# Performance work log

Hardware: AMD Instinct MI355X
Metric: run time of the kernel (lower is better)

Reference implementation:

```python
import jax, jax.numpy as jnp
import numpy as np

NUM_HEADS = 8
NUM_LEVEL = 4
KERNEL = 2
NUM_POINT = KERNEL * KERNEL
D_MODEL = 256
HEAD_DIM = D_MODEL // NUM_HEADS
REF_SIZE = 4
EPS = 1e-6


def _kernel_indices():
    # even kernel: linspace(-k/2+0.5, k/2-0.5, k) -> [-0.5, 0.5] for k=2
    ind = np.linspace(-KERNEL // 2 + 0.5, KERNEL // 2 - 0.5, KERNEL)
    i, j = np.meshgrid(ind, ind, indexing='ij')
    ki = np.stack([j, i], axis=-1).reshape(-1, 2) / KERNEL  # (P, 2), (x, y)
    return jnp.asarray(ki, dtype=jnp.float32)


def _ref_windows(shapes):
    # mask is None -> centers on a regular grid, size = ref_size / (H, W)
    refs = []
    for (H, W) in shapes:
        y = (jnp.arange(1, H + 1, dtype=jnp.float32) - 0.5) / (H + EPS)
        x = (jnp.arange(1, W + 1, dtype=jnp.float32) - 0.5) / (W + EPS)
        yy, xx = jnp.meshgrid(y, x, indexing='ij')           # (H, W)
        center = jnp.stack([xx, yy], axis=-1).reshape(-1, 2)  # (HW, 2)
        size = jnp.broadcast_to(
            jnp.array([REF_SIZE / W, REF_SIZE / H], dtype=jnp.float32), center.shape)
        refs.append(jnp.concatenate([center, size], axis=-1))
    return jnp.concatenate(refs, axis=0)  # (L, 4)


def _bilinear_sample(vflat, grid, H, W):
    """vflat: (B, H*W, M, D) one level; grid: (B, Lq, M, P, 2) normalized [0,1].
    Returns (B, Lq, M, P, D). Zero padding outside, align_corners=False."""
    B, _, M, D = vflat.shape
    x = grid[..., 0] * W - 0.5
    y = grid[..., 1] * H - 0.5
    x0 = jnp.floor(x); y0 = jnp.floor(y)
    lx = x - x0; ly = y - y0
    x0i = x0.astype(jnp.int32); y0i = y0.astype(jnp.int32)
    bidx = jnp.arange(B)[:, None, None, None]
    midx = jnp.arange(M)[None, None, :, None]

    def corner(xi, yi, w):
        valid = (xi >= 0) & (xi < W) & (yi >= 0) & (yi < H)
        idx = jnp.clip(yi, 0, H - 1) * W + jnp.clip(xi, 0, W - 1)
        g = vflat[bidx, idx, midx]  # (B, Lq, M, P, D)
        return g * (w * valid.astype(w.dtype))[..., None]

    out = corner(x0i, y0i, (1 - lx) * (1 - ly))
    out = out + corner(x0i + 1, y0i, lx * (1 - ly))
    out = out + corner(x0i, y0i + 1, (1 - lx) * ly)
    out = out + corner(x0i + 1, y0i + 1, lx * ly)
    return out


def setup_inputs() -> dict:
    key = jax.random.key(0)
    ks = jax.random.split(key, 20)
    spatial = [(100, 100), (50, 50), (25, 25), (13, 13)]
    B = 4
    inp = {}
    for i, (H, W) in enumerate(spatial):
        inp[f'value{i}'] = jax.random.normal(ks[i], (B, D_MODEL, H, W), dtype=jnp.float32)
        inp[f'pos{i}'] = jax.random.normal(ks[4 + i], (B, D_MODEL, H, W), dtype=jnp.float32)
    s = 0.05
    inp['Wv'] = jax.random.normal(ks[8], (D_MODEL, D_MODEL), dtype=jnp.float32) * s
    inp['bv'] = jnp.zeros((D_MODEL,), dtype=jnp.float32)
    inp['Wo'] = jax.random.normal(ks[9], (D_MODEL, D_MODEL), dtype=jnp.float32) * s
    inp['bo'] = jnp.zeros((D_MODEL,), dtype=jnp.float32)
    nb = NUM_LEVEL * NUM_HEADS * 4
    inp['Wbox'] = jax.random.normal(ks[10], (nb, D_MODEL), dtype=jnp.float32) * s
    inp['bbox'] = jax.random.uniform(ks[11], (nb,), dtype=jnp.float32)
    na = NUM_HEADS * NUM_LEVEL * NUM_POINT
    inp['Wattn'] = jax.random.normal(ks[12], (na, D_MODEL), dtype=jnp.float32) * s
    inp['battn'] = jax.random.normal(ks[13], (na,), dtype=jnp.float32) * s
    return inp


def reference(value0, value1, value2, value3, pos0, pos1, pos2, pos3,
              Wv, bv, Wo, bo, Wbox, bbox, Wattn, battn):
    levels = [value0, value1, value2, value3]
    poss = [pos0, pos1, pos2, pos3]
    shapes = [(v.shape[2], v.shape[3]) for v in levels]
    B = levels[0].shape[0]

    # flatten pyramid: (B, C, H, W) -> (B, HW, C)
    value = jnp.concatenate(
        [v.reshape(B, D_MODEL, -1).transpose(0, 2, 1) for v in levels], axis=1)
    pos = jnp.concatenate(
        [p.reshape(B, D_MODEL, -1).transpose(0, 2, 1) for p in poss], axis=1)
    L = value.shape[1]

    query = value + pos
    vp = (value @ Wv.T + bv).reshape(B, L, NUM_HEADS, HEAD_DIM)

    attn = jax.nn.softmax(
        (query @ Wattn.T + battn).reshape(B, L, NUM_HEADS, NUM_LEVEL * NUM_POINT),
        axis=-1).reshape(B, L, NUM_HEADS, NUM_LEVEL, NUM_POINT)

    offset = (query @ Wbox.T + bbox).reshape(B, L, NUM_HEADS, NUM_LEVEL, 4)
    ref = _ref_windows(shapes)[None, :, None, None, :]          # (1, L, 1, 1, 4)
    boxes = ref + offset / 8.0 * ref[..., jnp.array([2, 3, 2, 3])]
    center = boxes[..., None, :2]                               # (B, L, M, NL, 1, 2)
    size = boxes[..., None, 2:]
    ki = _kernel_indices()[None, None, None, None, :, :]        # (1,1,1,1,P,2)
    grid = center + ki * jax.nn.relu(size)                      # (B, L, M, NL, P, 2)

    out = jnp.zeros((B, L, NUM_HEADS, HEAD_DIM), dtype=vp.dtype)
    start = 0
    for l, (H, W) in enumerate(shapes):
        end = start + H * W
        vf = vp[:, start:end]                                   # (B, HW, M, D)
        sampled = _bilinear_sample(vf, grid[:, :, :, l], H, W)  # (B, L, M, P, D)
        out = out + jnp.einsum('blmp,blmpd->blmd', attn[:, :, :, l], sampled)
        start = end

    return out.reshape(B, L, D_MODEL) @ Wo.T + bo
```

## Files before the change

### kernel.cpp

```cpp
#include <hip/hip_runtime.h>
#include <cstdint>
#include <cmath>

#define D_MODEL 256
#define NH 8
#define NLVL 4
#define LTOT 13294
#define BATCH 4
#define BTOT (BATCH * LTOT)
#define RPAD 53248

typedef __attribute__((ext_vector_type(8))) short bf8;
typedef __attribute__((ext_vector_type(4))) float f4;
typedef __attribute__((ext_vector_type(2))) float f2;

__device__ __forceinline__ unsigned short f2bf(float x) {
    unsigned u = __float_as_uint(x);
    u += 0x7fffu + ((u >> 16) & 1u);
    return (unsigned short)(u >> 16);
}
__device__ __forceinline__ float bf2f(unsigned short h) {
    return __uint_as_float(((unsigned)h) << 16);
}
__device__ __forceinline__ f2 up2(unsigned u) {
    return (f2){__uint_as_float(u << 16), __uint_as_float(u & 0xffff0000u)};
}
__device__ __forceinline__ int swzf(int i, int s) { return s ^ ((i >> 1) & 3); }
__device__ __forceinline__ int xcd_swz(int hw, int nwg) {
    int xcd = hw & 7, k = hw >> 3;
    int q = nwg >> 3, r = nwg & 7;
    return (xcd < r ? xcd * (q + 1) : r * (q + 1) + (xcd - r) * q) + k;
}

__device__ __forceinline__ void level_of(int l, int& lv, int& hw, int& Wl, int& HWl, int& loff) {
    if (l < 10000)      { lv = 0; loff = 0;     Wl = 100; HWl = 10000; }
    else if (l < 12500) { lv = 1; loff = 10000; Wl = 50;  HWl = 2500;  }
    else if (l < 13125) { lv = 2; loff = 12500; Wl = 25;  HWl = 625;   }
    else                { lv = 3; loff = 13125; Wl = 13;  HWl = 169;   }
    hw = l - loff;
}

#define NCONV (RPAD / 64)
#define NPACK 96
#define NGEO  208

__global__ __launch_bounds__(256) void convert_pack(
    const float* __restrict__ v0, const float* __restrict__ v1,
    const float* __restrict__ v2, const float* __restrict__ v3,
    const float* __restrict__ p0, const float* __restrict__ p1,
    const float* __restrict__ p2, const float* __restrict__ p3,
    const float* __restrict__ Wv, const float* __restrict__ Wattn,
    const float* __restrict__ Wbox, const float* __restrict__ Wo,
    unsigned short* __restrict__ Gv, unsigned short* __restrict__ Gq,
    unsigned short* __restrict__ W1hi, unsigned short* __restrict__ W1lo,
    unsigned short* __restrict__ Wohi, unsigned short* __restrict__ Wolo,
    float4* __restrict__ geot) {
    __shared__ unsigned short HV[64][130];
    __shared__ unsigned short HQ[64][130];
    int t = threadIdx.x;

    if (blockIdx.x >= NCONV) {
        if (blockIdx.x >= NCONV + NPACK) {
            int rr = (blockIdx.x - (NCONV + NPACK)) * 256 + t;
            if (rr < BTOT) {
                int l = rr % LTOT;
                int lv, hw, Wl, HWl, loff;
                level_of(l, lv, hw, Wl, HWl, loff);
                int x, y;
                switch (lv) {
                    case 0:  y = hw / 100; x = hw - y * 100; break;
                    case 1:  y = hw / 50;  x = hw - y * 50;  break;
                    case 2:  y = hw / 25;  x = hw - y * 25;  break;
                    default: y = hw / 13;  x = hw - y * 13;  break;
                }
                float denom = (float)((double)Wl + 1e-6);
                float4 g;
                g.x = ((float)x + 0.5f) / denom;
                g.y = ((float)y + 0.5f) / denom;
                g.z = 4.0f / (float)Wl;
                g.w = __int_as_float(rr - l);
                geot[rr] = g;
            }
            return;
        }
        int tid = (blockIdx.x - NCONV) * 256 + t;
        const float* src;
        unsigned short *dh, *dl;
        int nb, kb, j, s;
        if (tid < 16384) {
            nb = tid >> 12; kb = (tid >> 9) & 7; j = (tid >> 2) & 127; s = tid & 3;
            int f = nb * 128 + j, c0 = kb * 32 + s * 8;
            if (f < 256)      src = Wv + (size_t)f * 256 + c0;
            else if (f < 384) src = Wattn + (size_t)(f - 256) * 256 + c0;
            else              src = Wbox + (size_t)(f - 384) * 256 + c0;
            dh = W1hi; dl = W1lo;
        } else {
            int t2 = tid - 16384;
            nb = t2 >> 12; kb = (t2 >> 9) & 7; j = (t2 >> 2) & 127; s = t2 & 3;
            int f = nb * 128 + j, c0 = kb * 32 + s * 8;
            src = Wo + (size_t)f * 256 + c0;
            dh = Wohi; dl = Wolo;
        }
        int base = (((nb * 8 + kb) * 128 + j) * 4 + swzf(j, s)) * 8;
        #pragma unroll
        for (int e = 0; e < 8; ++e) {
            float x = src[e];
            unsigned short h = f2bf(x);
            dh[base + e] = h;
            dl[base + e] = f2bf(x - bf2f(h));
        }
        return;
    }

    int w = t >> 6, lane = t & 63;
    int r0 = blockIdx.x * 64;

    int r = r0 + lane; if (r >= BTOT) r = BTOT - 1;
    int b = r / LTOT, l = r % LTOT;
    int lv, hw, Wl, HWl, loff;
    level_of(l, lv, hw, Wl, HWl, loff);
    const float *vb, *pb;
    switch (lv) { case 0: vb = v0; pb = p0; break; case 1: vb = v1; pb = p1; break;
                  case 2: vb = v2; pb = p2; break; default: vb = v3; pb = p3; break; }
    size_t base = (size_t)b * D_MODEL * (size_t)HWl + (size_t)hw;
    vb += base; pb += base;

    int kb2 = (lane >> 2) & 3, slot = lane & 3;
    for (int h = 0; h < 2; ++h) {
        #pragma unroll 4
        for (int i = 0; i < 32; ++i) {
            int cl = i * 4 + w;
            int c = h * 128 + cl;
            float av = vb[(size_t)c * HWl];
            float aq = av + pb[(size_t)c * HWl];
            HV[lane][cl] = f2bf(av);
            HQ[lane][cl] = f2bf(aq);
        }
        __syncthreads();
        #pragma unroll
        for (int j = 0; j < 8; ++j) {
            int plane = j >> 2;
            int rl = (j & 3) * 16 + w * 4 + (lane >> 4);
            int oct = slot ^ ((rl >> 1) & 3);
            const unsigned* s32 = (const unsigned*)(plane ? &HQ[rl][kb2 * 32 + oct * 8]
                                                          : &HV[rl][kb2 * 32 + oct * 8]);
            uint4 vst = make_uint4(s32[0], s32[1], s32[2], s32[3]);
            unsigned short* dst = (plane ? Gq : Gv)
                + (size_t)(r0 + rl) * 256 + (h * 4 + kb2) * 32 + slot * 8;
            *(uint4*)dst = vst;
        }
        __syncthreads();
    }
}

__global__ __launch_bounds__(512, 4) void gemm1_mfma(
    const unsigned short* __restrict__ Gv, const unsigned short* __restrict__ Gq,
    const unsigned short* __restrict__ W1hi, const unsigned short* __restrict__ W1lo,
    const float* __restrict__ bv, const float* __restrict__ battn, const float* __restrict__ bbox,
    unsigned short* __restrict__ VPb, float* __restrict__ LB) {
    __shared__ __align__(16) unsigned short Ah[2][8192], Bh[2][4096], Bl[2][4096];
    int t = threadIdx.x;
    int lid = xcd_swz(blockIdx.x, 4 * (RPAD / 256));
    int nb = lid & 3;
    int r0 = (lid >> 2) * 256;
    const unsigned short* Asrc = (nb < 2) ? Gv : Gq;
    int w = t >> 6, lane = t & 63;
    int wr = w >> 1, wc = w & 1;
    int row_l = lane & 15, oct = lane >> 4;

    const unsigned short* Bbh = W1hi + (size_t)nb * 32768;
    const unsigned short* Bbl = W1lo + (size_t)nb * 32768;

    f4 acc[4][4];
    #pragma unroll
    for (int i = 0; i < 4; ++i)
        #pragma unroll
        for (int j = 0; j < 4; ++j) acc[i][j] = (f4){0.f, 0.f, 0.f, 0.f};

    int c0 = t, c1 = t + 512;
    const unsigned short* a0b = Asrc + (size_t)(r0 + (c0 >> 2)) * 256 + (c0 & 3) * 8;
    const unsigned short* a1b = Asrc + (size_t)(r0 + (c1 >> 2)) * 256 + (c1 & 3) * 8;

#define G1_STAGE(bb, kb)                                                            \
    {                                                                               \
        __builtin_amdgcn_global_load_lds(a0b + (kb) * 32, &Ah[bb][w * 512], 16, 0, 0);        \
        __builtin_amdgcn_global_load_lds(a1b + (kb) * 32, &Ah[bb][4096 + w * 512], 16, 0, 0); \
        __builtin_amdgcn_global_load_lds(Bbh + (kb) * 4096 + c0 * 8, &Bh[bb][w * 512], 16, 0, 0); \
        __builtin_amdgcn_global_load_lds(Bbl + (kb) * 4096 + c0 * 8, &Bl[bb][w * 512], 16, 0, 0); \
    }

    G1_STAGE(0, 0);
    for (int kb = 0; kb < 8; ++kb) {
        __syncthreads();
        if (kb < 7) G1_STAGE((kb + 1) & 1, kb + 1);
        int bb = kb & 1;
        bf8 a[4], bh[4], bl[4];
        #pragma unroll
        for (int x = 0; x < 4; ++x) {
            int ri = wr * 64 + x * 16 + row_l;
            int ci = wc * 64 + x * 16 + row_l;
            a[x]  = *(const bf8*)(&Ah[bb][ri * 32 + swzf(ri, oct) * 8]);
            bh[x] = *(const bf8*)(&Bh[bb][ci * 32 + swzf(ci, oct) * 8]);
            bl[x] = *(const bf8*)(&Bl[bb][ci * 32 + swzf(ci, oct) * 8]);
        }
        #pragma unroll
        for (int mi = 0; mi < 4; ++mi)
            #pragma unroll
            for (int ni = 0; ni < 4; ++ni) {
                f4 c = acc[mi][ni];
                c = __builtin_amdgcn_mfma_f32_16x16x32_bf16(a[mi], bh[ni], c, 0, 0, 0);
                c = __builtin_amdgcn_mfma_f32_16x16x32_bf16(a[mi], bl[ni], c, 0, 0, 0);
                acc[mi][ni] = c;
            }
    }
    #pragma unroll
    for (int ni = 0; ni < 4; ++ni) {
        int col = wc * 64 + ni * 16 + row_l;
        float bias;
        if (nb == 0) bias = bv[col];
        else if (nb == 1) bias = bv[128 + col];
        else if (nb == 2) bias = battn[col];
        else bias = bbox[col];
        #pragma unroll
        for (int mi = 0; mi < 4; ++mi) {
            #pragma unroll
            for (int v = 0; v < 4; ++v) {
                int rr = r0 + wr * 64 + mi * 16 + oct * 4 + v;
                if (rr < BTOT) {
                    float val = acc[mi][ni][v] + bias;
                    if (nb < 2) VPb[(size_t)rr * 256 + nb * 128 + col] = f2bf(val);
                    else        LB[(size_t)rr * 256 + (nb - 2) * 128 + col] = val;
                }
            }
        }
    }
}

__global__ __launch_bounds__(256) void sampler_kernel(const unsigned short* __restrict__ VPb,
                                                      const float* __restrict__ LB,
                                                      const float4* __restrict__ geot,
                                                      unsigned short* __restrict__ att_hi,
                                                      unsigned short* __restrict__ att_lo) {
    __shared__ float sw[64][128];
    const int Ws2[4]   = {100, 50, 25, 13};
    const int offs2[4] = {0, 10000, 12500, 13125};
    int t = threadIdx.x;
    int blk = xcd_swz(blockIdx.x, (BTOT * NH) / 64);

    #pragma unroll
    for (int pass = 0; pass < 4; ++pass) {
        int g = (t >> 4) + pass * 16;
        int p = t & 15;
        int grp = blk * 64 + g;
        int m = grp & 7;
        int r = grp >> 3;

        float4 gt = geot[r];
        float cx = gt.x, cy = gt.y, rsw = gt.z;
        int rb0 = __float_as_int(gt.w);

        const float* Lrow = LB + (size_t)r * 256;
        float lg = Lrow[m * 16 + p];
        float mx = lg;
        #pragma unroll
        for (int off = 8; off >= 1; off >>= 1)
            mx = fmaxf(mx, __shfl_xor(mx, off, 16));
        float e = __expf(lg - mx);
        float ssum = e;
        #pragma unroll
        for (int off = 8; off >= 1; off >>= 1)
            ssum += __shfl_xor(ssum, off, 16);
        float aw = e / ssum;

        int lp = p >> 2, pp = p & 3;
        int W2 = Ws2[lp];
        float fW2 = (float)W2;
        float o0 = Lrow[128 + m * 16 + lp * 4 + 0];
        float o1 = Lrow[128 + m * 16 + lp * 4 + 1];
        float o2 = Lrow[128 + m * 16 + lp * 4 + 2];
        float o3 = Lrow[128 + m * 16 + lp * 4 + 3];
        float bcx = cx + o0 * 0.125f * rsw;
        float bcy = cy + o1 * 0.125f * rsw;
        float bsx = fmaxf(fmaf(o2 * 0.125f, rsw, rsw), 0.f);
        float bsy = fmaxf(fmaf(o3 * 0.125f, rsw, rsw), 0.f);
        float kx = (pp & 1)  ? 0.25f : -0.25f;
        float ky = (pp >> 1) ? 0.25f : -0.25f;
        float xs = fmaf(bcx + kx * bsx, fW2, -0.5f);
        float ys = fmaf(bcy + ky * bsy, fW2, -0.5f);
        float x0f = floorf(xs), y0f = floorf(ys);
        float lx = xs - x0f, ly = ys - y0f;
        int x0 = (int)x0f, y0 = (int)y0f;
        int x1 = x0 + 1, y1 = y0 + 1;
        bool vx0 = (x0 >= 0) & (x0 < W2), vx1 = (x1 >= 0) & (x1 < W2);
        bool vy0 = (y0 >= 0) & (y0 < W2), vy1 = (y1 >= 0) & (y1 < W2);
        int x0c = min(max(x0, 0), W2 - 1), x1c = min(max(x1, 0), W2 - 1);
        int y0c = min(max(y0, 0), W2 - 1), y1c = min(max(y1, 0), W2 - 1);
        float w00 = (vx0 & vy0) ? aw * (1.f - lx) * (1.f - ly) : 0.f;
        float w01 = (vx1 & vy0) ? aw * lx * (1.f - ly) : 0.f;
        float w10 = (vx0 & vy1) ? aw * (1.f - lx) * ly : 0.f;
        float w11 = (vx1 & vy1) ? aw * lx * ly : 0.f;
        int rowb = rb0 + offs2[lp];
        int col  = m * 32;
        int i00 = ((rowb + y0c * W2 + x0c) * 256 + col) * 2;
        int i01 = ((rowb + y0c * W2 + x1c) * 256 + col) * 2;
        int i10 = ((rowb + y1c * W2 + x0c) * 256 + col) * 2;
        int i11 = ((rowb + y1c * W2 + x1c) * 256 + col) * 2;
        float* dst = &sw[g][(p ^ (g & 3)) << 3];
        *(float4*)dst       = (float4){w00, w01, w10, w11};
        *(float4*)(dst + 4) = (float4){__int_as_float(i00), __int_as_float(i01),
                                       __int_as_float(i10), __int_as_float(i11)};
    }
    __syncthreads();

    int g = t >> 2, lane4 = t & 3;
    unsigned dby = (unsigned)lane4 * 16u;
    const char* Vb = (const char*)VPb;
    f2 a01 = {0.f, 0.f}, a23 = {0.f, 0.f}, a45 = {0.f, 0.f}, a67 = {0.f, 0.f};
    #pragma unroll
    for (int p = 0; p < 16; ++p) {
        const float* sp = &sw[g][(p ^ (g & 3)) << 3];
        float4 wv = *(const float4*)sp;
        float4 fi = *(const float4*)(sp + 4);
        uint4 u00 = *(const uint4*)(Vb + (size_t)(__float_as_uint(fi.x) + dby));
        uint4 u01 = *(const uint4*)(Vb + (size_t)(__float_as_uint(fi.y) + dby));
        uint4 u10 = *(const uint4*)(Vb + (size_t)(__float_as_uint(fi.z) + dby));
        uint4 u11 = *(const uint4*)(Vb + (size_t)(__float_as_uint(fi.w) + dby));
        f2 w0 = {wv.x, wv.x}, w1 = {wv.y, wv.y}, w2 = {wv.z, wv.z}, w3 = {wv.w, wv.w};
        a01 = __builtin_elementwise_fma(w0, up2(u00.x), a01);
        a23 = __builtin_elementwise_fma(w0, up2(u00.y), a23);
        a45 = __builtin_elementwise_fma(w0, up2(u00.z), a45);
        a67 = __builtin_elementwise_fma(w0, up2(u00.w), a67);
        a01 = __builtin_elementwise_fma(w1, up2(u01.x), a01);
        a23 = __builtin_elementwise_fma(w1, up2(u01.y), a23);
        a45 = __builtin_elementwise_fma(w1, up2(u01.z), a45);
        a67 = __builtin_elementwise_fma(w1, up2(u01.w), a67);
        a01 = __builtin_elementwise_fma(w2, up2(u10.x), a01);
        a23 = __builtin_elementwise_fma(w2, up2(u10.y), a23);
        a45 = __builtin_elementwise_fma(w2, up2(u10.z), a45);
        a67 = __builtin_elementwise_fma(w2, up2(u10.w), a67);
        a01 = __builtin_elementwise_fma(w3, up2(u11.x), a01);
        a23 = __builtin_elementwise_fma(w3, up2(u11.y), a23);
        a45 = __builtin_elementwise_fma(w3, up2(u11.z), a45);
        a67 = __builtin_elementwise_fma(w3, up2(u11.w), a67);
    }
    int grp = blk * 64 + g;
    int m2 = grp & 7, r2 = grp >> 3;
    int slot = lane4 ^ ((r2 >> 1) & 3);
    size_t base = (size_t)r2 * 256 + m2 * 32 + slot * 8;
    float av[8] = {a01.x, a01.y, a23.x, a23.y, a45.x, a45.y, a67.x, a67.y};
    unsigned hp[4], lp4[4];
    #pragma unroll
    for (int q = 0; q < 4; ++q) {
        unsigned short h0 = f2bf(av[q * 2]), h1 = f2bf(av[q * 2 + 1]);
        unsigned short l0 = f2bf(av[q * 2] - bf2f(h0)), l1 = f2bf(av[q * 2 + 1] - bf2f(h1));
        hp[q]  = ((unsigned)h1 << 16) | h0;
        lp4[q] = ((unsigned)l1 << 16) | l0;
    }
    *(uint4*)&att_hi[base] = make_uint4(hp[0], hp[1], hp[2], hp[3]);
    *(uint4*)&att_lo[base] = make_uint4(lp4[0], lp4[1], lp4[2], lp4[3]);
}

__global__ __launch_bounds__(512, 2) void gemm2_mfma(
    const unsigned short* __restrict__ Ahi_g, const unsigned short* __restrict__ Alo_g,
    const unsigned short* __restrict__ Wohi, const unsigned short* __restrict__ Wolo,
    const float* __restrict__ bo, float* __restrict__ out) {
    __shared__ __align__(16) unsigned short Ah[2][8192], Al[2][8192], Bh[2][4096], Bl[2][4096];
    int t = threadIdx.x;
    int lid = xcd_swz(blockIdx.x, 2 * (RPAD / 256));
    int nb = lid & 1;
    int r0 = (lid >> 1) * 256;
    int w = t >> 6, lane = t & 63;
    int wr = w >> 1, wc = w & 1;
    int row_l = lane & 15, oct = lane >> 4;

    const unsigned short* Bbh = Wohi + (size_t)nb * 32768;
    const unsigned short* Bbl = Wolo + (size_t)nb * 32768;

    f4 acc[4][4];
    #pragma unroll
    for (int i = 0; i < 4; ++i)
        #pragma unroll
        for (int j = 0; j < 4; ++j) acc[i][j] = (f4){0.f, 0.f, 0.f, 0.f};

    int c0 = t, c1 = t + 512;
    int ra0 = r0 + (c0 >> 2); if (ra0 >= BTOT) ra0 = BTOT - 1;
    int ra1 = r0 + (c1 >> 2); if (ra1 >= BTOT) ra1 = BTOT - 1;
    const unsigned short* ah0 = Ahi_g + (size_t)ra0 * 256 + (c0 & 3) * 8;
    const unsigned short* ah1 = Ahi_g + (size_t)ra1 * 256 + (c1 & 3) * 8;
    const unsigned short* al0 = Alo_g + (size_t)ra0 * 256 + (c0 & 3) * 8;
    const unsigned short* al1 = Alo_g + (size_t)ra1 * 256 + (c1 & 3) * 8;

#define G2_STAGE(bb, kb)                                                            \
    {                                                                               \
        __builtin_amdgcn_global_load_lds(ah0 + (kb) * 32, &Ah[bb][w * 512], 16, 0, 0);        \
        __builtin_amdgcn_global_load_lds(ah1 + (kb) * 32, &Ah[bb][4096 + w * 512], 16, 0, 0); \
        __builtin_amdgcn_global_load_lds(al0 + (kb) * 32, &Al[bb][w * 512], 16, 0, 0);        \
        __builtin_amdgcn_global_load_lds(al1 + (kb) * 32, &Al[bb][4096 + w * 512], 16, 0, 0); \
        __builtin_amdgcn_global_load_lds(Bbh + (kb) * 4096 + c0 * 8, &Bh[bb][w * 512], 16, 0, 0); \
        __builtin_amdgcn_global_load_lds(Bbl + (kb) * 4096 + c0 * 8, &Bl[bb][w * 512], 16, 0, 0); \
    }

    G2_STAGE(0, 0);
    for (int kb = 0; kb < 8; ++kb) {
        __syncthreads();
        if (kb < 7) G2_STAGE((kb + 1) & 1, kb + 1);
        int bb = kb & 1;
        bf8 ah[4], al[4], bh[4], bl[4];
        #pragma unroll
        for (int x = 0; x < 4; ++x) {
            int ri = wr * 64 + x * 16 + row_l;
            int ci = wc * 64 + x * 16 + row_l;
            ah[x] = *(const bf8*)(&Ah[bb][ri * 32 + swzf(ri, oct) * 8]);
            al[x] = *(const bf8*)(&Al[bb][ri * 32 + swzf(ri, oct) * 8]);
            bh[x] = *(const bf8*)(&Bh[bb][ci * 32 + swzf(ci, oct) * 8]);
            bl[x] = *(const bf8*)(&Bl[bb][ci * 32 + swzf(ci, oct) * 8]);
        }
        #pragma unroll
        for (int mi = 0; mi < 4; ++mi)
            #pragma unroll
            for (int ni = 0; ni < 4; ++ni) {
                f4 c = acc[mi][ni];
                c = __builtin_amdgcn_mfma_f32_16x16x32_bf16(ah[mi], bh[ni], c, 0, 0, 0);
                c = __builtin_amdgcn_mfma_f32_16x16x32_bf16(ah[mi], bl[ni], c, 0, 0, 0);
                c = __builtin_amdgcn_mfma_f32_16x16x32_bf16(al[mi], bh[ni], c, 0, 0, 0);
                acc[mi][ni] = c;
            }
    }
    #pragma unroll
    for (int ni = 0; ni < 4; ++ni) {
        int col = wc * 64 + ni * 16 + row_l;
        float bias = bo[nb * 128 + col];
        #pragma unroll
        for (int mi = 0; mi < 4; ++mi) {
            #pragma unroll
            for (int v = 0; v < 4; ++v) {
                int rr = r0 + wr * 64 + mi * 16 + oct * 4 + v;
                if (rr < BTOT)
                    out[(size_t)rr * 256 + nb * 128 + col] = acc[mi][ni][v] + bias;
            }
        }
    }
}

extern "C" void kernel_launch(void* const* d_in, const int* in_sizes, int n_in,
                              void* d_out, int out_size, void* d_ws, size_t ws_size,
                              hipStream_t stream) {
    const float* v0 = (const float*)d_in[0];
    const float* p0 = (const float*)d_in[1];
    const float* v1 = (const float*)d_in[2];
    const float* p1 = (const float*)d_in[3];
    const float* v2 = (const float*)d_in[4];
    const float* p2 = (const float*)d_in[5];
    const float* v3 = (const float*)d_in[6];
    const float* p3 = (const float*)d_in[7];
    const float* Wv    = (const float*)d_in[8];
    const float* bv    = (const float*)d_in[9];
    const float* Wo    = (const float*)d_in[10];
    const float* bo    = (const float*)d_in[11];
    const float* Wbox  = (const float*)d_in[12];
    const float* bbox  = (const float*)d_in[13];
    const float* Wattn = (const float*)d_in[14];
    const float* battn = (const float*)d_in[15];
    float* out = (float*)d_out;

    char* ws = (char*)d_ws;
    unsigned short* W1hi = (unsigned short*)(ws);
    unsigned short* W1lo = (unsigned short*)(ws + 262144);
    unsigned short* Wohi = (unsigned short*)(ws + 524288);
    unsigned short* Wolo = (unsigned short*)(ws + 655360);
    unsigned short* Gv   = (unsigned short*)(ws + 1048576);
    unsigned short* Gq   = (unsigned short*)(ws + 1048576 + 27262976);
    unsigned short* atth = Gv;
    unsigned short* attl = Gq;
    unsigned short* VPb  = (unsigned short*)(ws + 1048576 + 2 * 27262976);
    float*          LB   = (float*)(ws + 1048576 + 2 * 27262976 + 27226112);
    float4*         geot = (float4*)(ws + 1048576 + 2 * 27262976 + 27226112 + 54452224);

    convert_pack<<<dim3(NCONV + NPACK + NGEO), dim3(256), 0, stream>>>(
        v0, v1, v2, v3, p0, p1, p2, p3, Wv, Wattn, Wbox, Wo,
        Gv, Gq, W1hi, W1lo, Wohi, Wolo, geot);

    gemm1_mfma<<<dim3(4 * (RPAD / 256)), dim3(512), 0, stream>>>(
        Gv, Gq, W1hi, W1lo, bv, battn, bbox, VPb, LB);

    sampler_kernel<<<dim3((BTOT * NH) / 64), dim3(256), 0, stream>>>(VPb, LB, geot, atth, attl);

    gemm2_mfma<<<dim3(2 * (RPAD / 256)), dim3(512), 0, stream>>>(
        atth, attl, Wohi, Wolo, bo, out);
}
```

Before: 211.7 us.

## Replace LDS staging in sampler with per-lane level compute and lane shuffles

```diff
diff --git a/kernel.cpp b/kernel.cpp
--- a/kernel.cpp
+++ b/kernel.cpp
@@ -241,48 +241,45 @@
                                                       const float4* __restrict__ geot,
                                                       unsigned short* __restrict__ att_hi,
                                                       unsigned short* __restrict__ att_lo) {
-    __shared__ float sw[64][128];
-    const int Ws2[4]   = {100, 50, 25, 13};
-    const int offs2[4] = {0, 10000, 12500, 13125};
     int t = threadIdx.x;
     int blk = xcd_swz(blockIdx.x, (BTOT * NH) / 64);
-
-    #pragma unroll
-    for (int pass = 0; pass < 4; ++pass) {
-        int g = (t >> 4) + pass * 16;
-        int p = t & 15;
-        int grp = blk * 64 + g;
-        int m = grp & 7;
-        int r = grp >> 3;
-
-        float4 gt = geot[r];
-        float cx = gt.x, cy = gt.y, rsw = gt.z;
-        int rb0 = __float_as_int(gt.w);
-
-        const float* Lrow = LB + (size_t)r * 256;
-        float lg = Lrow[m * 16 + p];
-        float mx = lg;
-        #pragma unroll
-        for (int off = 8; off >= 1; off >>= 1)
-            mx = fmaxf(mx, __shfl_xor(mx, off, 16));
-        float e = __expf(lg - mx);
-        float ssum = e;
-        #pragma unroll
-        for (int off = 8; off >= 1; off >>= 1)
-            ssum += __shfl_xor(ssum, off, 16);
-        float aw = e / ssum;
-
-        int lp = p >> 2, pp = p & 3;
-        int W2 = Ws2[lp];
-        float fW2 = (float)W2;
-        float o0 = Lrow[128 + m * 16 + lp * 4 + 0];
-        float o1 = Lrow[128 + m * 16 + lp * 4 + 1];
-        float o2 = Lrow[128 + m * 16 + lp * 4 + 2];
-        float o3 = Lrow[128 + m * 16 + lp * 4 + 3];
-        float bcx = cx + o0 * 0.125f * rsw;
-        float bcy = cy + o1 * 0.125f * rsw;
-        float bsx = fmaxf(fmaf(o2 * 0.125f, rsw, rsw), 0.f);
-        float bsy = fmaxf(fmaf(o3 * 0.125f, rsw, rsw), 0.f);
+    int gidx = t >> 2, lane4 = t & 3;
+    int grp = blk * 64 + gidx;
+    int m = grp & 7, r = grp >> 3;
+
+    float4 gt = geot[r];
+    float cx = gt.x, cy = gt.y, rsw = gt.z;
+    int rb0 = __float_as_int(gt.w);
+
+    const float* Lrow = LB + (size_t)r * 256;
+    float4 lg4 = *(const float4*)&Lrow[m * 16 + lane4 * 4];
+    float4 ob  = *(const float4*)&Lrow[128 + m * 16 + lane4 * 4];
+
+    float mx = fmaxf(fmaxf(lg4.x, lg4.y), fmaxf(lg4.z, lg4.w));
+    mx = fmaxf(mx, __shfl_xor(mx, 1, 4));
+    mx = fmaxf(mx, __shfl_xor(mx, 2, 4));
+    float e0 = __expf(lg4.x - mx), e1 = __expf(lg4.y - mx);
+    float e2 = __expf(lg4.z - mx), e3 = __expf(lg4.w - mx);
+    float s = (e0 + e1) + (e2 + e3);
+    s += __shfl_xor(s, 1, 4);
+    s += __shfl_xor(s, 2, 4);
+    float inv = 1.0f / s;
+
+    float fW2 = lane4 == 0 ? 100.f : lane4 == 1 ? 50.f : lane4 == 2 ? 25.f : 13.f;
+    int   W2i = lane4 == 0 ? 100   : lane4 == 1 ? 50   : lane4 == 2 ? 25   : 13;
+    int  rowb = rb0 + (lane4 == 0 ? 0 : lane4 == 1 ? 10000 : lane4 == 2 ? 12500 : 13125);
+    int  col  = m * 32;
+
+    float bcx = cx + ob.x * 0.125f * rsw;
+    float bcy = cy + ob.y * 0.125f * rsw;
+    float bsx = fmaxf(fmaf(ob.z * 0.125f, rsw, rsw), 0.f);
+    float bsy = fmaxf(fmaf(ob.w * 0.125f, rsw, rsw), 0.f);
+
+    float4 wA[4]; int4 iA[4];
+    float ev[4] = {e0, e1, e2, e3};
+    #pragma unroll
+    for (int pp = 0; pp < 4; ++pp) {
+        float aw = ev[pp] * inv;
         float kx = (pp & 1)  ? 0.25f : -0.25f;
         float ky = (pp >> 1) ? 0.25f : -0.25f;
         float xs = fmaf(bcx + kx * bsx, fW2, -0.5f);
@@ -291,62 +288,65 @@
         float lx = xs - x0f, ly = ys - y0f;
         int x0 = (int)x0f, y0 = (int)y0f;
         int x1 = x0 + 1, y1 = y0 + 1;
-        bool vx0 = (x0 >= 0) & (x0 < W2), vx1 = (x1 >= 0) & (x1 < W2);
-        bool vy0 = (y0 >= 0) & (y0 < W2), vy1 = (y1 >= 0) & (y1 < W2);
-        int x0c = min(max(x0, 0), W2 - 1), x1c = min(max(x1, 0), W2 - 1);
-        int y0c = min(max(y0, 0), W2 - 1), y1c = min(max(y1, 0), W2 - 1);
-        float w00 = (vx0 & vy0) ? aw * (1.f - lx) * (1.f - ly) : 0.f;
-        float w01 = (vx1 & vy0) ? aw * lx * (1.f - ly) : 0.f;
-        float w10 = (vx0 & vy1) ? aw * (1.f - lx) * ly : 0.f;
-        float w11 = (vx1 & vy1) ? aw * lx * ly : 0.f;
-        int rowb = rb0 + offs2[lp];
-        int col  = m * 32;
-        int i00 = ((rowb + y0c * W2 + x0c) * 256 + col) * 2;
-        int i01 = ((rowb + y0c * W2 + x1c) * 256 + col) * 2;
-        int i10 = ((rowb + y1c * W2 + x0c) * 256 + col) * 2;
-        int i11 = ((rowb + y1c * W2 + x1c) * 256 + col) * 2;
-        float* dst = &sw[g][(p ^ (g & 3)) << 3];
-        *(float4*)dst       = (float4){w00, w01, w10, w11};
-        *(float4*)(dst + 4) = (float4){__int_as_float(i00), __int_as_float(i01),
-                                       __int_as_float(i10), __int_as_float(i11)};
-    }
-    __syncthreads();
-
-    int g = t >> 2, lane4 = t & 3;
+        bool vx0 = (x0 >= 0) & (x0 < W2i), vx1 = (x1 >= 0) & (x1 < W2i);
+        bool vy0 = (y0 >= 0) & (y0 < W2i), vy1 = (y1 >= 0) & (y1 < W2i);
+        int x0c = min(max(x0, 0), W2i - 1), x1c = min(max(x1, 0), W2i - 1);
+        int y0c = min(max(y0, 0), W2i - 1), y1c = min(max(y1, 0), W2i - 1);
+        wA[pp].x = (vx0 & vy0) ? aw * (1.f - lx) * (1.f - ly) : 0.f;
+        wA[pp].y = (vx1 & vy0) ? aw * lx * (1.f - ly) : 0.f;
+        wA[pp].z = (vx0 & vy1) ? aw * (1.f - lx) * ly : 0.f;
+        wA[pp].w = (vx1 & vy1) ? aw * lx * ly : 0.f;
+        iA[pp].x = ((rowb + y0c * W2i + x0c) * 256 + col) * 2;
+        iA[pp].y = ((rowb + y0c * W2i + x1c) * 256 + col) * 2;
+        iA[pp].z = ((rowb + y1c * W2i + x0c) * 256 + col) * 2;
+        iA[pp].w = ((rowb + y1c * W2i + x1c) * 256 + col) * 2;
+    }
+
     unsigned dby = (unsigned)lane4 * 16u;
     const char* Vb = (const char*)VPb;
     f2 a01 = {0.f, 0.f}, a23 = {0.f, 0.f}, a45 = {0.f, 0.f}, a67 = {0.f, 0.f};
-    #pragma unroll
-    for (int p = 0; p < 16; ++p) {
-        const float* sp = &sw[g][(p ^ (g & 3)) << 3];
-        float4 wv = *(const float4*)sp;
-        float4 fi = *(const float4*)(sp + 4);
-        uint4 u00 = *(const uint4*)(Vb + (size_t)(__float_as_uint(fi.x) + dby));
-        uint4 u01 = *(const uint4*)(Vb + (size_t)(__float_as_uint(fi.y) + dby));
-        uint4 u10 = *(const uint4*)(Vb + (size_t)(__float_as_uint(fi.z) + dby));
-        uint4 u11 = *(const uint4*)(Vb + (size_t)(__float_as_uint(fi.w) + dby));
-        f2 w0 = {wv.x, wv.x}, w1 = {wv.y, wv.y}, w2 = {wv.z, wv.z}, w3 = {wv.w, wv.w};
-        a01 = __builtin_elementwise_fma(w0, up2(u00.x), a01);
-        a23 = __builtin_elementwise_fma(w0, up2(u00.y), a23);
-        a45 = __builtin_elementwise_fma(w0, up2(u00.z), a45);
-        a67 = __builtin_elementwise_fma(w0, up2(u00.w), a67);
-        a01 = __builtin_elementwise_fma(w1, up2(u01.x), a01);
-        a23 = __builtin_elementwise_fma(w1, up2(u01.y), a23);
-        a45 = __builtin_elementwise_fma(w1, up2(u01.z), a45);
-        a67 = __builtin_elementwise_fma(w1, up2(u01.w), a67);
-        a01 = __builtin_elementwise_fma(w2, up2(u10.x), a01);
-        a23 = __builtin_elementwise_fma(w2, up2(u10.y), a23);
-        a45 = __builtin_elementwise_fma(w2, up2(u10.z), a45);
-        a67 = __builtin_elementwise_fma(w2, up2(u10.w), a67);
-        a01 = __builtin_elementwise_fma(w3, up2(u11.x), a01);
-        a23 = __builtin_elementwise_fma(w3, up2(u11.y), a23);
-        a45 = __builtin_elementwise_fma(w3, up2(u11.z), a45);
-        a67 = __builtin_elementwise_fma(w3, up2(u11.w), a67);
-    }
-    int grp = blk * 64 + g;
-    int m2 = grp & 7, r2 = grp >> 3;
-    int slot = lane4 ^ ((r2 >> 1) & 3);
-    size_t base = (size_t)r2 * 256 + m2 * 32 + slot * 8;
+
+#define PSTEP(P)                                                                      \
+    {                                                                                 \
+        float w00 = __shfl(wA[(P) & 3].x, (P) >> 2, 4);                               \
+        float w01 = __shfl(wA[(P) & 3].y, (P) >> 2, 4);                               \
+        float w10 = __shfl(wA[(P) & 3].z, (P) >> 2, 4);                               \
+        float w11 = __shfl(wA[(P) & 3].w, (P) >> 2, 4);                               \
+        unsigned o00 = (unsigned)__shfl(iA[(P) & 3].x, (P) >> 2, 4) + dby;            \
+        unsigned o01 = (unsigned)__shfl(iA[(P) & 3].y, (P) >> 2, 4) + dby;            \
+        unsigned o10 = (unsigned)__shfl(iA[(P) & 3].z, (P) >> 2, 4) + dby;            \
+        unsigned o11 = (unsigned)__shfl(iA[(P) & 3].w, (P) >> 2, 4) + dby;            \
+        uint4 u00 = *(const uint4*)(Vb + (size_t)o00);                                \
+        uint4 u01 = *(const uint4*)(Vb + (size_t)o01);                                \
+        uint4 u10 = *(const uint4*)(Vb + (size_t)o10);                                \
+        uint4 u11 = *(const uint4*)(Vb + (size_t)o11);                                \
+        f2 ww0 = {w00, w00}, ww1 = {w01, w01}, ww2 = {w10, w10}, ww3 = {w11, w11};    \
+        a01 = __builtin_elementwise_fma(ww0, up2(u00.x), a01);                        \
+        a23 = __builtin_elementwise_fma(ww0, up2(u00.y), a23);                        \
+        a45 = __builtin_elementwise_fma(ww0, up2(u00.z), a45);                        \
+        a67 = __builtin_elementwise_fma(ww0, up2(u00.w), a67);                        \
+        a01 = __builtin_elementwise_fma(ww1, up2(u01.x), a01);                        \
+        a23 = __builtin_elementwise_fma(ww1, up2(u01.y), a23);                        \
+        a45 = __builtin_elementwise_fma(ww1, up2(u01.z), a45);                        \
+        a67 = __builtin_elementwise_fma(ww1, up2(u01.w), a67);                        \
+        a01 = __builtin_elementwise_fma(ww2, up2(u10.x), a01);                        \
+        a23 = __builtin_elementwise_fma(ww2, up2(u10.y), a23);                        \
+        a45 = __builtin_elementwise_fma(ww2, up2(u10.z), a45);                        \
+        a67 = __builtin_elementwise_fma(ww2, up2(u10.w), a67);                        \
+        a01 = __builtin_elementwise_fma(ww3, up2(u11.x), a01);                        \
+        a23 = __builtin_elementwise_fma(ww3, up2(u11.y), a23);                        \
+        a45 = __builtin_elementwise_fma(ww3, up2(u11.z), a45);                        \
+        a67 = __builtin_elementwise_fma(ww3, up2(u11.w), a67);                        \
+    }
+
+    PSTEP(0)  PSTEP(1)  PSTEP(2)  PSTEP(3)
+    PSTEP(4)  PSTEP(5)  PSTEP(6)  PSTEP(7)
+    PSTEP(8)  PSTEP(9)  PSTEP(10) PSTEP(11)
+    PSTEP(12) PSTEP(13) PSTEP(14) PSTEP(15)
+#undef PSTEP
+
+    int slot = lane4 ^ ((r >> 1) & 3);
+    size_t base = (size_t)r * 256 + m * 32 + slot * 8;
     float av[8] = {a01.x, a01.y, a23.x, a23.y, a45.x, a45.y, a67.x, a67.y};
     unsigned hp[4], lp4[4];
     #pragma unroll
```

Measured after the change: 209.5 us, median of 3. About the same (-1.0%).
